# Performance work log

Measured on AMD Instinct MI355X. Metric: run time of the kernel, lower is better.

Reference implementation:

```python
import jax, jax.numpy as jnp
import numpy as np

B, Fc, C, H, D, L = 128, 256, 256, 8, 32, 6  # batch, columns, dim, heads, head_dim, layers


def _ln(x, g, b, eps=1e-5):
    m = x.mean(-1, keepdims=True)
    v = ((x - m) ** 2).mean(-1, keepdims=True)
    return (x - m) * jax.lax.rsqrt(v + eps) * g + b


def setup_inputs() -> dict:
    key = jax.random.key(0)
    ks = jax.random.split(key, 16)
    s = 0.02  # weight init scale to keep 6-layer activations stable
    return {
        "x": jax.random.normal(ks[0], (B, Fc, C), jnp.float32),
        "col_emb": jax.random.normal(ks[1], (1, Fc, C), jnp.float32),
        "pos_emb": jax.random.normal(ks[2], (1, Fc + 1, C), jnp.float32),
        "col_bias": jax.random.normal(ks[3], (Fc, Fc), jnp.float32),
        "ln1_g": jnp.ones((L, C), jnp.float32),
        "ln1_b": jnp.zeros((L, C), jnp.float32),
        "qkv_w": jax.random.normal(ks[4], (L, C, 3 * C), jnp.float32) * s,
        "qkv_b": jnp.zeros((L, 3 * C), jnp.float32),
        "out_w": jax.random.normal(ks[5], (L, C, C), jnp.float32) * s,
        "out_b": jnp.zeros((L, C), jnp.float32),
        "ln2_g": jnp.ones((L, C), jnp.float32),
        "ln2_b": jnp.zeros((L, C), jnp.float32),
        "w1": jax.random.normal(ks[6], (L, C, 4 * C), jnp.float32) * s,
        "b1": jnp.zeros((L, 4 * C), jnp.float32),
        "w2": jax.random.normal(ks[7], (L, 4 * C, 2 * C), jnp.float32) * s,
        "b2": jnp.zeros((L, 2 * C), jnp.float32),
        "w3": jax.random.normal(ks[8], (L, C, C), jnp.float32) * s,
        "b3": jnp.zeros((L, C), jnp.float32),
        "fin_g": jnp.ones((C,), jnp.float32),
        "fin_b": jnp.zeros((C,), jnp.float32),
    }


def reference(x, col_emb, pos_emb, col_bias, ln1_g, ln1_b, qkv_w, qkv_b,
              out_w, out_b, ln2_g, ln2_b, w1, b1, w2, b2, w3, b3, fin_g, fin_b):
    Fdim = x.shape[1]
    h = x + col_emb[:, :Fdim] + pos_emb[:, 1:Fdim + 1]
    bias = col_bias[:Fdim, :Fdim]  # [T, T]
    scale = 1.0 / np.sqrt(D).astype(np.float32)
    params = (ln1_g, ln1_b, qkv_w, qkv_b, out_w, out_b, ln2_g, ln2_b,
              w1, b1, w2, b2, w3, b3)

    def block(xc, p):
        g1, be1, qw, qb, ow, ob, g2, be2, W1, B1, W2, B2, W3, B3 = p
        Bn, T, Cd = xc.shape
        hn = _ln(xc, g1, be1)
        qkv = hn @ qw + qb                              # [B,T,3C]
        q, k, v = jnp.split(qkv, 3, axis=-1)
        q = q.reshape(Bn, T, H, D)
        k = k.reshape(Bn, T, H, D)
        v = v.reshape(Bn, T, H, D)
        scores = jnp.einsum('bthd,bshd->bhts', q, k) * scale + bias[None, None]
        w = jax.nn.softmax(scores, axis=-1)             # dropout = identity (eval)
        attn = jnp.einsum('bhts,bshd->bthd', w, v).reshape(Bn, T, Cd)
        attn = attn @ ow + ob
        attn = attn + bias[None]                        # [1,T,T] broadcast, T==C
        xc = xc + attn
        hn2 = _ln(xc, g2, be2)
        u = jax.nn.gelu(hn2 @ W1 + B1, approximate=False)
        gl = u @ W2 + B2                                # [B,T,2C]
        a, gate = jnp.split(gl, 2, axis=-1)
        xc = xc + (a * jax.nn.sigmoid(gate)) @ W3 + B3
        return xc, None

    h, _ = jax.lax.scan(block, h, params)
    h = _ln(h, fin_g, fin_b)
    return h.mean(axis=1)  # pooling='mean' -> [B, C]
```

## Files before the change

### kernel.cpp

```cpp
#include <hip/hip_runtime.h>

typedef __bf16 bx8 __attribute__((ext_vector_type(8)));
typedef float fx4 __attribute__((ext_vector_type(4)));

#define GAS(p) ((const __attribute__((address_space(1))) void*)(const void*)(p))
#define LAS(p) ((__attribute__((address_space(3))) void*)(void*)(p))

__device__ __forceinline__ unsigned short f2bf(float f) {
  return __builtin_bit_cast(unsigned short, (__bf16)f);
}
__device__ __forceinline__ float bf2f(unsigned short s) {
  unsigned u = ((unsigned)s) << 16;
  return __builtin_bit_cast(float, u);
}

__global__ __launch_bounds__(256) void wtrans_kernel(const float* __restrict__ src,
                                                     unsigned short* __restrict__ dst,
                                                     int K, int N) {
  __shared__ unsigned short t[64][68];
  const int l = blockIdx.z;
  const float* s = src + (size_t)l * K * N;
  unsigned short* d = dst + (size_t)l * N * K;
  const int n0 = blockIdx.x * 64, k0 = blockIdx.y * 64;
  const int tx = threadIdx.x & 63, ty = threadIdx.x >> 6;
#pragma unroll
  for (int r = 0; r < 64; r += 4)
    t[tx][ty + r] = f2bf(s[(size_t)(k0 + ty + r) * N + n0 + tx]);
  __syncthreads();
#pragma unroll
  for (int r = 0; r < 64; r += 4)
    d[(size_t)(n0 + ty + r) * K + k0 + tx] = t[ty + r][tx];
}

__global__ __launch_bounds__(256) void embed_kernel(const float4* __restrict__ x,
                                                    const float4* __restrict__ ce,
                                                    const float4* __restrict__ pe,
                                                    float4* __restrict__ o) {
  int i = blockIdx.x * 256 + threadIdx.x;
  int c4 = i & 63;
  int t = (i >> 6) & 255;
  float4 a = x[i], b = ce[t * 64 + c4], p = pe[(t + 1) * 64 + c4];
  o[i] = make_float4(a.x + b.x + p.x, a.y + b.y + p.y, a.z + b.z + p.z, a.w + b.w + p.w);
}

template <int MODE>
__global__ __launch_bounds__(256) void ln_kernel(const float* __restrict__ x,
                                                 const float* __restrict__ gw,
                                                 const float* __restrict__ bw,
                                                 unsigned short* __restrict__ out,
                                                 float2* __restrict__ stats) {
  int row = blockIdx.x * 4 + (threadIdx.x >> 6);
  int lane = threadIdx.x & 63;
  const float4 v = *(const float4*)(x + (size_t)row * 256 + lane * 4);
  float s = v.x + v.y + v.z + v.w;
  float q = v.x * v.x + v.y * v.y + v.z * v.z + v.w * v.w;
#pragma unroll
  for (int off = 1; off < 64; off <<= 1) {
    s += __shfl_xor(s, off);
    q += __shfl_xor(q, off);
  }
  float mean = s * (1.0f / 256.0f);
  float rs = rsqrtf(q * (1.0f / 256.0f) - mean * mean + 1e-5f);
  if (MODE == 1) {
    if (lane == 0) stats[row] = make_float2(mean, rs);
    return;
  }
  float4 gv = *(const float4*)(gw + lane * 4);
  float4 bv = *(const float4*)(bw + lane * 4);
  ushort4 o;
  o.x = f2bf((v.x - mean) * rs * gv.x + bv.x);
  o.y = f2bf((v.y - mean) * rs * gv.y + bv.y);
  o.z = f2bf((v.z - mean) * rs * gv.z + bv.z);
  o.w = f2bf((v.w - mean) * rs * gv.w + bv.w);
  *(ushort4*)(out + (size_t)row * 256 + lane * 4) = o;
}

__global__ __launch_bounds__(256) void swiglu_kernel(const unsigned short* __restrict__ gl,
                                                     unsigned short* __restrict__ g) {
  int i = blockIdx.x * 256 + threadIdx.x;
  int m = i >> 6;
  int c4 = (i & 63) * 4;
  const ushort4 a = *(const ushort4*)(gl + (size_t)m * 512 + c4);
  const ushort4 gt = *(const ushort4*)(gl + (size_t)m * 512 + 256 + c4);
  ushort4 o;
  o.x = f2bf(bf2f(a.x) / (1.0f + __expf(-bf2f(gt.x))));
  o.y = f2bf(bf2f(a.y) / (1.0f + __expf(-bf2f(gt.y))));
  o.z = f2bf(bf2f(a.z) / (1.0f + __expf(-bf2f(gt.z))));
  o.w = f2bf(bf2f(a.w) / (1.0f + __expf(-bf2f(gt.w))));
  *(ushort4*)(g + (size_t)m * 256 + c4) = o;
}

__global__ __launch_bounds__(256) void mean_part_kernel(const float* __restrict__ x,
                                                        const float2* __restrict__ stats,
                                                        float* __restrict__ part) {
  int b = blockIdx.x, half = blockIdx.y, c = threadIdx.x;
  const float* xb = x + (size_t)b * 65536 + half * 32768;
  const float2* st = stats + b * 256 + half * 128;
  float acc = 0.f;
#pragma unroll 4
  for (int t = 0; t < 128; ++t) {
    float2 s = st[t];
    acc += (xb[t * 256 + c] - s.x) * s.y;
  }
  part[(size_t)(b * 2 + half) * 256 + c] = acc;
}
__global__ __launch_bounds__(256) void mean_fin_kernel(const float* __restrict__ part,
                                                       const float* __restrict__ fg,
                                                       const float* __restrict__ fb,
                                                       float* __restrict__ out) {
  int b = blockIdx.x, c = threadIdx.x;
  out[b * 256 + c] =
      (part[(size_t)(2 * b) * 256 + c] + part[(size_t)(2 * b + 1) * 256 + c]) *
          (1.0f / 256.0f) * fg[c] + fb[c];
}

template <int EP>
__global__ __launch_bounds__(256) void gemm_kernel(const unsigned short* __restrict__ A,
                                                   const unsigned short* __restrict__ BT,
                                                   const float* __restrict__ bvec,
                                                   const float* __restrict__ cbias,
                                                   float* __restrict__ resid,
                                                   unsigned short* __restrict__ outb,
                                                   int N, int K) {
  __shared__ unsigned short lA[2][128 * 32];
  __shared__ unsigned short lB[2][128 * 32];
  const int tid = threadIdx.x;
  const int lane = tid & 63, w = tid >> 6;
  const int wr = w >> 1, wc = w & 1;
  const int g = lane >> 4, lr = lane & 15;
  const int m0 = blockIdx.y * 128, n0 = blockIdx.x * 128;
  fx4 acc[4][4] = {};

  auto STAGE = [&](int buf, int kk) {
#pragma unroll
    for (int r = 0; r < 2; ++r) {
      int u = r * 256 + tid;
      int row = u >> 2, sl = u & 3;
      int c = sl ^ ((row >> 1) & 3);
      __builtin_amdgcn_global_load_lds(GAS(A + (size_t)(m0 + row) * K + kk + c * 8),
                                       LAS(&lA[buf][u * 8]), 16, 0, 0);
      __builtin_amdgcn_global_load_lds(GAS(BT + (size_t)(n0 + row) * K + kk + c * 8),
                                       LAS(&lB[buf][u * 8]), 16, 0, 0);
    }
  };
  auto COMPUTE = [&](int buf) {
    bx8 af[4], bq[4];
#pragma unroll
    for (int i = 0; i < 4; ++i) {
      int row = wr * 64 + i * 16 + lr;
      af[i] = *(const bx8*)&lA[buf][row * 32 + (g ^ ((row >> 1) & 3)) * 8];
      int col = wc * 64 + i * 16 + lr;
      bq[i] = *(const bx8*)&lB[buf][col * 32 + (g ^ ((col >> 1) & 3)) * 8];
    }
#pragma unroll
    for (int i = 0; i < 4; ++i)
#pragma unroll
      for (int j = 0; j < 4; ++j)
        acc[i][j] = __builtin_amdgcn_mfma_f32_16x16x32_bf16(bq[j], af[i], acc[i][j], 0, 0, 0);
  };

  STAGE(0, 0);
  asm volatile("s_waitcnt vmcnt(0)" ::: "memory");
  __syncthreads();
  int cur = 0;
  const int nt = K >> 5;
  for (int t2 = 1; t2 < nt; ++t2) {
    STAGE(cur ^ 1, t2 * 32);
    COMPUTE(cur);
    __syncthreads();
    cur ^= 1;
  }
  COMPUTE(cur);

#pragma unroll
  for (int i = 0; i < 4; ++i) {
    const int m = m0 + wr * 64 + i * 16 + lr;
#pragma unroll
    for (int j = 0; j < 4; ++j) {
      const int nc = n0 + wc * 64 + j * 16 + g * 4;
      const float4 bv = *(const float4*)(bvec + nc);
      float v0 = acc[i][j][0] + bv.x, v1 = acc[i][j][1] + bv.y;
      float v2 = acc[i][j][2] + bv.z, v3 = acc[i][j][3] + bv.w;
      if constexpr (EP == 1) {
        v0 = 0.5f * v0 * (1.0f + erff(v0 * 0.70710678118654752f));
        v1 = 0.5f * v1 * (1.0f + erff(v1 * 0.70710678118654752f));
        v2 = 0.5f * v2 * (1.0f + erff(v2 * 0.70710678118654752f));
        v3 = 0.5f * v3 * (1.0f + erff(v3 * 0.70710678118654752f));
      }
      if constexpr (EP == 0 || EP == 1) {
        ushort4 st;
        st.x = f2bf(v0); st.y = f2bf(v1); st.z = f2bf(v2); st.w = f2bf(v3);
        *(ushort4*)(outb + (size_t)m * N + nc) = st;
      } else if constexpr (EP == 2 || EP == 3) {
        if constexpr (EP == 2) {
          const float4 cb = *(const float4*)(cbias + (size_t)(m & 255) * 256 + nc);
          v0 += cb.x; v1 += cb.y; v2 += cb.z; v3 += cb.w;
        }
        float4* rp = (float4*)(resid + (size_t)m * N + nc);
        float4 old = *rp;
        *rp = make_float4(old.x + v0, old.y + v1, old.z + v2, old.w + v3);
      } else {
        if (nc < 512) {
          ushort4 st;
          st.x = f2bf(v0); st.y = f2bf(v1); st.z = f2bf(v2); st.w = f2bf(v3);
          *(ushort4*)(outb + (size_t)m * N + nc) = st;
        } else {
          unsigned short* vTp = (unsigned short*)resid;
          const int s = m & 255, b = m >> 8;
          const int hv = nc - 512;
          const int h = hv >> 5, d0 = hv & 31;
          const int jj = (s & 3) + 4 * ((s >> 4) & 1);
          const int ub = (s >> 5) * 128 + ((s >> 2) & 3) * 32 + d0;
          unsigned short* base = vTp + (size_t)(b * 8 + h) * 8192;
          const float vv[4] = {v0, v1, v2, v3};
#pragma unroll
          for (int r = 0; r < 4; ++r) {
            int u = ub + r;
            int up = (u & ~7) | ((u & 7) ^ ((u >> 3) & 7));
            base[up * 8 + jj] = f2bf(vv[r]);
          }
        }
      }
    }
  }
}

__global__ __launch_bounds__(256) void attn_kernel(const unsigned short* __restrict__ qkv,
                                                   const unsigned short* __restrict__ vT,
                                                   const float* __restrict__ cbias,
                                                   unsigned short* __restrict__ attnb) {
  __shared__ unsigned short Kl[256 * 32];
  __shared__ unsigned short Vl[1024 * 8];
  const int bh = blockIdx.x, b = bh >> 3, h = bh & 7;
  const int tid = threadIdx.x, lane = tid & 63, w = tid >> 6;
  const int g = lane >> 4, lr = lane & 15;
  const unsigned short* qb_ = qkv + (size_t)b * 196608;
  const unsigned short* vTb = vT + (size_t)bh * 8192;
#pragma unroll
  for (int r = 0; r < 4; ++r) {
    int u = r * 256 + tid;
    int s = u >> 2, sl = u & 3;
    int c = sl ^ ((s >> 1) & 3);
    __builtin_amdgcn_global_load_lds(GAS(qb_ + (size_t)s * 768 + 256 + h * 32 + c * 8),
                                     LAS(&Kl[u * 8]), 16, 0, 0);
    __builtin_amdgcn_global_load_lds(GAS(vTb + u * 8), LAS(&Vl[u * 8]), 16, 0, 0);
  }
  asm volatile("s_waitcnt vmcnt(0)" ::: "memory");
  __syncthreads();
  const float scale = 0.17677669529663689f;
  const fx4 zero = {0.f, 0.f, 0.f, 0.f};
#pragma unroll 1
  for (int it = 0; it < 4; ++it) {
    const int t = it * 64 + w * 16 + lr;
    bx8 qf = *(const bx8*)(qb_ + (size_t)t * 768 + h * 32 + g * 8);
    float p[16][4];
    float mx = -1e30f;
#pragma unroll
    for (int n = 0; n < 16; ++n) {
      int sr = n * 16 + lr;
      bx8 kf = *(const bx8*)&Kl[sr * 32 + (g ^ ((sr >> 1) & 3)) * 8];
      fx4 sc = __builtin_amdgcn_mfma_f32_16x16x32_bf16(kf, qf, zero, 0, 0, 0);
      const float4 cb = *(const float4*)(cbias + (size_t)t * 256 + n * 16 + g * 4);
      p[n][0] = sc[0] * scale + cb.x;
      p[n][1] = sc[1] * scale + cb.y;
      p[n][2] = sc[2] * scale + cb.z;
      p[n][3] = sc[3] * scale + cb.w;
      mx = fmaxf(mx, fmaxf(fmaxf(p[n][0], p[n][1]), fmaxf(p[n][2], p[n][3])));
    }
    mx = fmaxf(mx, __shfl_xor(mx, 16));
    mx = fmaxf(mx, __shfl_xor(mx, 32));
    float sum = 0.f;
    bx8 bq[8];
#pragma unroll
    for (int c = 0; c < 8; ++c) {
      union { bx8 v; unsigned short u[8]; } pk;
#pragma unroll
      for (int jj = 0; jj < 8; ++jj) {
        float e = __expf(p[2 * c + (jj >> 2)][jj & 3] - mx);
        sum += e;
        pk.u[jj] = f2bf(e);
      }
      bq[c] = pk.v;
    }
    sum += __shfl_xor(sum, 16);
    sum += __shfl_xor(sum, 32);
    const float inv = 1.0f / sum;
    fx4 oa0 = zero, oa1 = zero;
#pragma unroll
    for (int c = 0; c < 8; ++c) {
      int u0 = c * 128 + g * 32 + lr;
      int u0p = (u0 & ~7) | ((u0 & 7) ^ ((u0 >> 3) & 7));
      bx8 vf0 = *(const bx8*)&Vl[u0p * 8];
      oa0 = __builtin_amdgcn_mfma_f32_16x16x32_bf16(vf0, bq[c], oa0, 0, 0, 0);
      int u1 = u0 + 16;
      int u1p = (u1 & ~7) | ((u1 & 7) ^ ((u1 >> 3) & 7));
      bx8 vf1 = *(const bx8*)&Vl[u1p * 8];
      oa1 = __builtin_amdgcn_mfma_f32_16x16x32_bf16(vf1, bq[c], oa1, 0, 0, 0);
    }
    ushort4 o0, o1;
    o0.x = f2bf(oa0[0] * inv); o0.y = f2bf(oa0[1] * inv);
    o0.z = f2bf(oa0[2] * inv); o0.w = f2bf(oa0[3] * inv);
    o1.x = f2bf(oa1[0] * inv); o1.y = f2bf(oa1[1] * inv);
    o1.z = f2bf(oa1[2] * inv); o1.w = f2bf(oa1[3] * inv);
    unsigned short* orow = attnb + (size_t)(b * 256 + t) * 256 + h * 32;
    *(ushort4*)(orow + 4 * g) = o0;
    *(ushort4*)(orow + 16 + 4 * g) = o1;
  }
}

extern "C" void kernel_launch(void* const* d_in, const int* in_sizes, int n_in,
                              void* d_out, int out_size, void* d_ws, size_t ws_size,
                              hipStream_t stream) {
  (void)in_sizes; (void)n_in; (void)out_size; (void)ws_size;
  const float* x     = (const float*)d_in[0];
  const float* cemb  = (const float*)d_in[1];
  const float* pemb  = (const float*)d_in[2];
  const float* cbias = (const float*)d_in[3];
  const float* ln1g  = (const float*)d_in[4];
  const float* ln1b  = (const float*)d_in[5];
  const float* qkvw  = (const float*)d_in[6];
  const float* qkvb  = (const float*)d_in[7];
  const float* outw  = (const float*)d_in[8];
  const float* outbv = (const float*)d_in[9];
  const float* ln2g  = (const float*)d_in[10];
  const float* ln2b  = (const float*)d_in[11];
  const float* w1    = (const float*)d_in[12];
  const float* b1    = (const float*)d_in[13];
  const float* w2    = (const float*)d_in[14];
  const float* b2    = (const float*)d_in[15];
  const float* w3    = (const float*)d_in[16];
  const float* b3    = (const float*)d_in[17];
  const float* fing  = (const float*)d_in[18];
  const float* finb  = (const float*)d_in[19];

  char* ws = (char*)d_ws;
  float* x_res = (float*)(ws);
  unsigned short* hn   = (unsigned short*)(ws + 33554432);
  unsigned short* big  = (unsigned short*)(ws + 50331648);
  unsigned short* glc  = (unsigned short*)(ws + 83886080);
  unsigned short* vT   = (unsigned short*)(ws + 100663296);
  unsigned short* wT   = (unsigned short*)(ws + 117440512);
  float2* stats = (float2*)(ws + 130809856);
  float* part  = (float*)big;

  unsigned short* qkvwT = wT;
  unsigned short* outwT = wT + 1179648;
  unsigned short* w1T   = wT + 1572864;
  unsigned short* w2T   = wT + 3145728;
  unsigned short* w3T   = wT + 6291456;

  wtrans_kernel<<<dim3(12, 4, 6), 256, 0, stream>>>(qkvw, qkvwT, 256, 768);
  wtrans_kernel<<<dim3(4, 4, 6), 256, 0, stream>>>(outw, outwT, 256, 256);
  wtrans_kernel<<<dim3(16, 4, 6), 256, 0, stream>>>(w1, w1T, 256, 1024);
  wtrans_kernel<<<dim3(8, 16, 6), 256, 0, stream>>>(w2, w2T, 1024, 512);
  wtrans_kernel<<<dim3(4, 4, 6), 256, 0, stream>>>(w3, w3T, 256, 256);
  embed_kernel<<<8192, 256, 0, stream>>>((const float4*)x, (const float4*)cemb,
                                         (const float4*)pemb, (float4*)x_res);
  for (int l = 0; l < 6; ++l) {
    ln_kernel<0><<<8192, 256, 0, stream>>>(x_res, ln1g + l * 256, ln1b + l * 256, hn, nullptr);
    gemm_kernel<4><<<dim3(6, 256), 256, 0, stream>>>(hn, qkvwT + (size_t)l * 196608,
                                                     qkvb + l * 768, nullptr, (float*)vT,
                                                     big, 768, 256);
    attn_kernel<<<1024, 256, 0, stream>>>(big, vT, cbias, hn);
    gemm_kernel<2><<<dim3(2, 256), 256, 0, stream>>>(hn, outwT + (size_t)l * 65536,
                                                     outbv + l * 256, cbias, x_res, nullptr,
                                                     256, 256);
    ln_kernel<0><<<8192, 256, 0, stream>>>(x_res, ln2g + l * 256, ln2b + l * 256, hn, nullptr);
    for (int c = 0; c < 2; ++c) {
      const size_t ro = (size_t)c * 16384 * 256;
      gemm_kernel<1><<<dim3(8, 128), 256, 0, stream>>>(hn + ro, w1T + (size_t)l * 262144,
                                                       b1 + l * 1024, nullptr, nullptr, big,
                                                       1024, 256);
      gemm_kernel<0><<<dim3(4, 128), 256, 0, stream>>>(big, w2T + (size_t)l * 524288,
                                                       b2 + l * 512, nullptr, nullptr, glc,
                                                       512, 1024);
      swiglu_kernel<<<4096, 256, 0, stream>>>(glc, hn + ro);
      gemm_kernel<3><<<dim3(2, 128), 256, 0, stream>>>(hn + ro, w3T + (size_t)l * 65536,
                                                       b3 + l * 256, nullptr, x_res + ro,
                                                       nullptr, 256, 256);
    }
  }
  ln_kernel<1><<<8192, 256, 0, stream>>>(x_res, nullptr, nullptr, nullptr, stats);
  mean_part_kernel<<<dim3(128, 2), 256, 0, stream>>>(x_res, stats, part);
  mean_fin_kernel<<<128, 256, 0, stream>>>(part, fing, finb, (float*)d_out);
}
```

Before: 1.740 ms.

## Fuse SwiGLU into W2 GEMM epilogue and drop MLP row chunking

Adds a dedicated W2 GEMM kernel in which each block computes matching tiles of both the value half and the gate half of the output. It applies bias and a*sigmoid(gate) in registers before writing bf16, which removes the separate swiglu kernel and the round trip of the 512-wide intermediate through global memory. The MLP is no longer split into two row chunks, so each GEMM launches once over all rows with a larger grid. In exchange the fused kernel holds twice the accumulators and three LDS tiles, which may reduce occupancy. The larger intermediate buffer now extends up to the transposed-weight region.

```diff
diff --git a/kernel.cpp b/kernel.cpp
--- a/kernel.cpp
+++ b/kernel.cpp
@@ -73,21 +73,6 @@
   o.z = f2bf((v.z - mean) * rs * gv.z + bv.z);
   o.w = f2bf((v.w - mean) * rs * gv.w + bv.w);
   *(ushort4*)(out + (size_t)row * 256 + lane * 4) = o;
-}
-
-__global__ __launch_bounds__(256) void swiglu_kernel(const unsigned short* __restrict__ gl,
-                                                     unsigned short* __restrict__ g) {
-  int i = blockIdx.x * 256 + threadIdx.x;
-  int m = i >> 6;
-  int c4 = (i & 63) * 4;
-  const ushort4 a = *(const ushort4*)(gl + (size_t)m * 512 + c4);
-  const ushort4 gt = *(const ushort4*)(gl + (size_t)m * 512 + 256 + c4);
-  ushort4 o;
-  o.x = f2bf(bf2f(a.x) / (1.0f + __expf(-bf2f(gt.x))));
-  o.y = f2bf(bf2f(a.y) / (1.0f + __expf(-bf2f(gt.y))));
-  o.z = f2bf(bf2f(a.z) / (1.0f + __expf(-bf2f(gt.z))));
-  o.w = f2bf(bf2f(a.w) / (1.0f + __expf(-bf2f(gt.w))));
-  *(ushort4*)(g + (size_t)m * 256 + c4) = o;
 }
 
 __global__ __launch_bounds__(256) void mean_part_kernel(const float* __restrict__ x,
@@ -225,6 +210,89 @@
   }
 }
 
+__global__ __launch_bounds__(256) void gemm_w2f_kernel(const unsigned short* __restrict__ A,
+                                                       const unsigned short* __restrict__ BT,
+                                                       const float* __restrict__ b2,
+                                                       unsigned short* __restrict__ gout) {
+  __shared__ unsigned short lA[2][128 * 32];
+  __shared__ unsigned short lBa[2][128 * 32];
+  __shared__ unsigned short lBg[2][128 * 32];
+  const int tid = threadIdx.x;
+  const int lane = tid & 63, w = tid >> 6;
+  const int wr = w >> 1, wc = w & 1;
+  const int g = lane >> 4, lr = lane & 15;
+  const int m0 = blockIdx.y * 128, n0 = blockIdx.x * 128;
+  fx4 aA[4][4] = {}, aG[4][4] = {};
+
+  auto STAGE = [&](int buf, int kk) {
+#pragma unroll
+    for (int r = 0; r < 2; ++r) {
+      int u = r * 256 + tid;
+      int row = u >> 2, sl = u & 3;
+      int c = sl ^ ((row >> 1) & 3);
+      __builtin_amdgcn_global_load_lds(GAS(A + (size_t)(m0 + row) * 1024 + kk + c * 8),
+                                       LAS(&lA[buf][u * 8]), 16, 0, 0);
+      __builtin_amdgcn_global_load_lds(GAS(BT + (size_t)(n0 + row) * 1024 + kk + c * 8),
+                                       LAS(&lBa[buf][u * 8]), 16, 0, 0);
+      __builtin_amdgcn_global_load_lds(GAS(BT + (size_t)(256 + n0 + row) * 1024 + kk + c * 8),
+                                       LAS(&lBg[buf][u * 8]), 16, 0, 0);
+    }
+  };
+  auto COMPUTE = [&](int buf) {
+    bx8 af[4], ba[4], bg[4];
+#pragma unroll
+    for (int i = 0; i < 4; ++i) {
+      int row = wr * 64 + i * 16 + lr;
+      int sw = (g ^ ((row >> 1) & 3)) * 8;
+      af[i] = *(const bx8*)&lA[buf][row * 32 + sw];
+      int col = wc * 64 + i * 16 + lr;
+      int swb = (g ^ ((col >> 1) & 3)) * 8;
+      ba[i] = *(const bx8*)&lBa[buf][col * 32 + swb];
+      bg[i] = *(const bx8*)&lBg[buf][col * 32 + swb];
+    }
+#pragma unroll
+    for (int i = 0; i < 4; ++i)
+#pragma unroll
+      for (int j = 0; j < 4; ++j) {
+        aA[i][j] = __builtin_amdgcn_mfma_f32_16x16x32_bf16(ba[j], af[i], aA[i][j], 0, 0, 0);
+        aG[i][j] = __builtin_amdgcn_mfma_f32_16x16x32_bf16(bg[j], af[i], aG[i][j], 0, 0, 0);
+      }
+  };
+
+  STAGE(0, 0);
+  asm volatile("s_waitcnt vmcnt(0)" ::: "memory");
+  __syncthreads();
+  int cur = 0;
+  for (int t2 = 1; t2 < 32; ++t2) {
+    STAGE(cur ^ 1, t2 * 32);
+    COMPUTE(cur);
+    __syncthreads();
+    cur ^= 1;
+  }
+  COMPUTE(cur);
+
+#pragma unroll
+  for (int i = 0; i < 4; ++i) {
+    const int m = m0 + wr * 64 + i * 16 + lr;
+#pragma unroll
+    for (int j = 0; j < 4; ++j) {
+      const int nc = n0 + wc * 64 + j * 16 + g * 4;
+      const float4 bva = *(const float4*)(b2 + nc);
+      const float4 bvg = *(const float4*)(b2 + 256 + nc);
+      float a0 = aA[i][j][0] + bva.x, a1 = aA[i][j][1] + bva.y;
+      float a2 = aA[i][j][2] + bva.z, a3 = aA[i][j][3] + bva.w;
+      float g0 = aG[i][j][0] + bvg.x, g1 = aG[i][j][1] + bvg.y;
+      float g2 = aG[i][j][2] + bvg.z, g3 = aG[i][j][3] + bvg.w;
+      ushort4 st;
+      st.x = f2bf(a0 / (1.0f + __expf(-g0)));
+      st.y = f2bf(a1 / (1.0f + __expf(-g1)));
+      st.z = f2bf(a2 / (1.0f + __expf(-g2)));
+      st.w = f2bf(a3 / (1.0f + __expf(-g3)));
+      *(ushort4*)(gout + (size_t)m * 256 + nc) = st;
+    }
+  }
+}
+
 __global__ __launch_bounds__(256) void attn_kernel(const unsigned short* __restrict__ qkv,
                                                    const unsigned short* __restrict__ vT,
                                                    const float* __restrict__ cbias,
@@ -337,7 +405,6 @@
   float* x_res = (float*)(ws);
   unsigned short* hn   = (unsigned short*)(ws + 33554432);
   unsigned short* big  = (unsigned short*)(ws + 50331648);
-  unsigned short* glc  = (unsigned short*)(ws + 83886080);
   unsigned short* vT   = (unsigned short*)(ws + 100663296);
   unsigned short* wT   = (unsigned short*)(ws + 117440512);
   float2* stats = (float2*)(ws + 130809856);
@@ -366,19 +433,14 @@
                                                      outbv + l * 256, cbias, x_res, nullptr,
                                                      256, 256);
     ln_kernel<0><<<8192, 256, 0, stream>>>(x_res, ln2g + l * 256, ln2b + l * 256, hn, nullptr);
-    for (int c = 0; c < 2; ++c) {
-      const size_t ro = (size_t)c * 16384 * 256;
-      gemm_kernel<1><<<dim3(8, 128), 256, 0, stream>>>(hn + ro, w1T + (size_t)l * 262144,
-                                                       b1 + l * 1024, nullptr, nullptr, big,
-                                                       1024, 256);
-      gemm_kernel<0><<<dim3(4, 128), 256, 0, stream>>>(big, w2T + (size_t)l * 524288,
-                                                       b2 + l * 512, nullptr, nullptr, glc,
-                                                       512, 1024);
-      swiglu_kernel<<<4096, 256, 0, stream>>>(glc, hn + ro);
-      gemm_kernel<3><<<dim3(2, 128), 256, 0, stream>>>(hn + ro, w3T + (size_t)l * 65536,
-                                                       b3 + l * 256, nullptr, x_res + ro,
-                                                       nullptr, 256, 256);
-    }
+    gemm_kernel<1><<<dim3(8, 256), 256, 0, stream>>>(hn, w1T + (size_t)l * 262144,
+                                                     b1 + l * 1024, nullptr, nullptr, big,
+                                                     1024, 256);
+    gemm_w2f_kernel<<<dim3(2, 256), 256, 0, stream>>>(big, w2T + (size_t)l * 524288,
+                                                      b2 + l * 512, hn);
+    gemm_kernel<3><<<dim3(2, 256), 256, 0, stream>>>(hn, w3T + (size_t)l * 65536,
+                                                     b3 + l * 256, nullptr, x_res, nullptr,
+                                                     256, 256);
   }
   ln_kernel<1><<<8192, 256, 0, stream>>>(x_res, nullptr, nullptr, nullptr, stats);
   mean_part_kernel<<<dim3(128, 2), 256, 0, stream>>>(x_res, stats, part);
```

Result: no change. 1.746 ms (+0.3%).
